# Optimization experiments

Measured on AMD Instinct MI355X. Metric: run time of the kernel, lower is better.

Reference implementation:

```python
import jax, jax.numpy as jnp
import numpy as np

B, S, D, H = 2, 2048, 1024, 16
HD = D // H  # head_dim = 64
SCALE = HD ** -0.5


def setup_inputs() -> dict:
    key = jax.random.key(0)
    ks = jax.random.split(key, 10)
    std = D ** -0.5
    return {
        "x": jax.random.normal(ks[0], (B, S, D), jnp.float32),
        "y": jax.random.normal(ks[1], (B, S, D), jnp.float32),
        "Wq": jax.random.normal(ks[2], (D, D), jnp.float32) * std,
        "bq": jnp.zeros((D,), jnp.float32),
        "Wk": jax.random.normal(ks[3], (D, D), jnp.float32) * std,
        "bk": jnp.zeros((D,), jnp.float32),
        "Wv": jax.random.normal(ks[4], (D, D), jnp.float32) * std,
        "bv": jnp.zeros((D,), jnp.float32),
        "Wo": jax.random.normal(ks[5], (D, D), jnp.float32) * std,
        "bo": jnp.zeros((D,), jnp.float32),
    }


def reference(x, y, Wq, bq, Wk, bk, Wv, bv, Wo, bo):
    # Linear projections (torch Linear: x @ W.T + b; here W stored as [in,out])
    q = x @ Wq + bq  # [B,S,D]
    k = y @ Wk + bk
    v = y @ Wv + bv
    # split heads -> [B,H,S,hd]
    q = q.reshape(B, S, H, HD).transpose(0, 2, 1, 3)
    k = k.reshape(B, S, H, HD).transpose(0, 2, 1, 3)
    v = v.reshape(B, S, H, HD).transpose(0, 2, 1, 3)
    scores = jnp.einsum("bhqd,bhkd->bhqk", q, k) * SCALE  # [B,H,S,S]
    causal = jnp.tril(jnp.ones((S, S), dtype=bool))  # keep lower triangle
    scores = jnp.where(causal[None, None], scores, -jnp.inf)
    attn = jax.nn.softmax(scores, axis=-1)
    out = jnp.einsum("bhqk,bhkd->bhqd", attn, v)  # [B,H,S,hd]
    out = out.transpose(0, 2, 1, 3).reshape(B, S, D)
    return out @ Wo + bo
```

## Files before the change

### kernel.cpp

```cpp
#include <hip/hip_runtime.h>
#include <hip/hip_bf16.h>


#define BDIM 2
#define SDIM 2048
#define DDIM 1024
#define HDIM 16
#define HD   64
#define MDIM (BDIM*SDIM)
#define C2 0.18033688011112042f

using short8  = __attribute__((ext_vector_type(8))) short;
using floatx4 = __attribute__((ext_vector_type(4))) float;

static __device__ __forceinline__ unsigned short f2bf(float x) {
    union { float f; unsigned int u; } c; c.f = x;
    unsigned int r = (c.u + 0x7fffu + ((c.u >> 16) & 1u)) >> 16;
    return (unsigned short)r;
}

static __device__ __forceinline__ unsigned int pack2bf(float a, float b) {
    union { float f; unsigned int u; } ua, ub;
    ua.f = a; ub.f = b;
    return __builtin_amdgcn_perm(ub.u + 0x8000u, ua.u + 0x8000u, 0x07060302u);
}

#define GLD16(g, l) __builtin_amdgcn_global_load_lds(                        \
    (const __attribute__((address_space(1))) void*)(g),                      \
    (__attribute__((address_space(3))) void*)(l), 16, 0, 0)

__global__ __launch_bounds__(256) void prep_kernel(
    const float* __restrict__ X, const float* __restrict__ Y,
    const float* __restrict__ W0, const float* __restrict__ W1,
    const float* __restrict__ W2, const float* __restrict__ W3,
    unsigned short* __restrict__ Xo, unsigned short* __restrict__ Yo,
    unsigned short* __restrict__ T0, unsigned short* __restrict__ T1,
    unsigned short* __restrict__ T2, unsigned short* __restrict__ T3)
{
    __shared__ float tile[64][68];
    const int z = blockIdx.z;
    const int t = threadIdx.x;
    if (z < 2) {
        const float* A    = z ? Y : X;
        unsigned short* O = z ? Yo : Xo;
        const int idx = blockIdx.x * 256 + t;
        const float4 a = ((const float4*)A)[idx*2];
        const float4 b = ((const float4*)A)[idx*2 + 1];
        ushort4 lo, hi;
        lo.x = f2bf(a.x); lo.y = f2bf(a.y); lo.z = f2bf(a.z); lo.w = f2bf(a.w);
        hi.x = f2bf(b.x); hi.y = f2bf(b.y); hi.z = f2bf(b.z); hi.w = f2bf(b.w);
        ((ushort4*)O)[idx*2]     = lo;
        ((ushort4*)O)[idx*2 + 1] = hi;
        return;
    }
    if (blockIdx.x >= 256) return;
    const int zz = z - 2;
    const float* W    = (zz == 0) ? W0 : (zz == 1) ? W1 : (zz == 2) ? W2 : W3;
    unsigned short* T = (zz == 0) ? T0 : (zz == 1) ? T1 : (zz == 2) ? T2 : T3;
    const int k0 = (blockIdx.x & 15) * 64, n0 = (blockIdx.x >> 4) * 64;
    #pragma unroll
    for (int i = 0; i < 4; ++i) {
        const int idx = t + i*256;
        const int kr = idx >> 4, c4 = idx & 15;
        float4 v = *(const float4*)&W[(size_t)(k0 + kr) * DDIM + n0 + c4*4];
        tile[kr][c4*4+0] = v.x; tile[kr][c4*4+1] = v.y;
        tile[kr][c4*4+2] = v.z; tile[kr][c4*4+3] = v.w;
    }
    __syncthreads();
    #pragma unroll
    for (int i = 0; i < 4; ++i) {
        const int idx = t + i*256;
        const int nr = idx >> 4, kc = idx & 15;
        ushort4 o;
        o.x = f2bf(tile[kc*4+0][nr]); o.y = f2bf(tile[kc*4+1][nr]);
        o.z = f2bf(tile[kc*4+2][nr]); o.w = f2bf(tile[kc*4+3][nr]);
        *(ushort4*)&T[(size_t)(n0 + nr) * DDIM + k0 + kc*4] = o;
    }
}

template <bool SWAP>
__device__ __forceinline__ void gemm128_core(
    const unsigned short* __restrict__ A, const unsigned short* __restrict__ Bt,
    int bm, int bn, unsigned short* As, unsigned short* Bs, floatx4 acc[4][4])
{
    const int t = threadIdx.x;
    const int w = t >> 6, l = t & 63;
    const int quad = l >> 4, col = l & 15;
    const int wr = (w >> 1) * 64, wc = (w & 1) * 64;

    const int c1 = t + 256;
    const int r0 = t >> 2,  o0 = (t & 3) * 8;
    const int r1 = c1 >> 2, o1 = (c1 & 3) * 8;

    const unsigned short* Ar0 = A  + (size_t)(bm + r0) * DDIM + o0;
    const unsigned short* Ar1 = A  + (size_t)(bm + r1) * DDIM + o1;
    const unsigned short* Br0 = Bt + (size_t)(bn + r0) * DDIM + o0;
    const unsigned short* Br1 = Bt + (size_t)(bn + r1) * DDIM + o1;

    GLD16(Ar0, As + t*8);
    GLD16(Ar1, As + c1*8);
    GLD16(Br0, Bs + t*8);
    GLD16(Br1, Bs + c1*8);

    for (int kt = 0; kt < DDIM; kt += 32) {
        const int cur = (kt >> 5) & 1;
        unsigned short* Asn = As + (cur ^ 1) * 4096;
        unsigned short* Bsn = Bs + (cur ^ 1) * 4096;
        __syncthreads();
        if (kt + 32 < DDIM) {
            GLD16(Ar0 + kt + 32, Asn + t*8);
            GLD16(Ar1 + kt + 32, Asn + c1*8);
            GLD16(Br0 + kt + 32, Bsn + t*8);
            GLD16(Br1 + kt + 32, Bsn + c1*8);
        }
        const unsigned short* Asc = As + cur*4096;
        const unsigned short* Bsc = Bs + cur*4096;
        short8 af[4], bfr[4];
        #pragma unroll
        for (int i = 0; i < 4; ++i)
            af[i] = *(const short8*)&Asc[(wr + i*16 + col)*32 + quad*8];
        #pragma unroll
        for (int j = 0; j < 4; ++j)
            bfr[j] = *(const short8*)&Bsc[(wc + j*16 + col)*32 + quad*8];
        #pragma unroll
        for (int i = 0; i < 4; ++i)
            #pragma unroll
            for (int j = 0; j < 4; ++j)
                acc[i][j] = SWAP
                    ? __builtin_amdgcn_mfma_f32_16x16x32_bf16(bfr[j], af[i], acc[i][j], 0, 0, 0)
                    : __builtin_amdgcn_mfma_f32_16x16x32_bf16(af[i], bfr[j], acc[i][j], 0, 0, 0);
    }
}

__global__ __launch_bounds__(256) void qkv_gemm_kernel(
    const unsigned short* __restrict__ xbf, const unsigned short* __restrict__ ybf,
    const unsigned short* __restrict__ Wqt, const unsigned short* __restrict__ Wkt,
    const unsigned short* __restrict__ Wvt,
    const float* __restrict__ bq, const float* __restrict__ bk,
    const float* __restrict__ bv,
    unsigned short* __restrict__ Qbf, unsigned short* __restrict__ Kbf,
    unsigned short* __restrict__ vT)
{
    __shared__ __align__(16) unsigned short As[2*4096];
    __shared__ __align__(16) unsigned short Bs[2*4096];

    const int z = blockIdx.z;
    const unsigned short* A  = (z == 0) ? xbf : ybf;
    const unsigned short* Wt = (z == 0) ? Wqt : (z == 1) ? Wkt : Wvt;
    const float* bp          = (z == 0) ? bq  : (z == 1) ? bk  : bv;

    const int bm = (blockIdx.x * 4 + (blockIdx.y & 3)) * 128;
    const int bn = (blockIdx.y >> 2) * 128;

    const int t = threadIdx.x;
    const int w = t >> 6, l = t & 63;
    const int quad = l >> 4, col = l & 15;
    const int wr = (w >> 1) * 64, wc = (w & 1) * 64;

    floatx4 acc[4][4] = {};

    if (z < 2) {
        gemm128_core<true>(A, Wt, bm, bn, As, Bs, acc);
        unsigned short* O = (z == 0) ? Qbf : Kbf;
        const float sc = (z == 0) ? C2 : 1.0f;
        float4 bias4[4];
        #pragma unroll
        for (int j = 0; j < 4; ++j)
            bias4[j] = *(const float4*)&bp[bn + wc + j*16 + quad*4];
        #pragma unroll
        for (int i = 0; i < 4; ++i) {
            const int m = bm + wr + i*16 + col;
            unsigned short* rowp = O + (size_t)m * DDIM;
            #pragma unroll
            for (int j = 0; j < 4; ++j) {
                const float v0 = (acc[i][j][0] + bias4[j].x) * sc;
                const float v1 = (acc[i][j][1] + bias4[j].y) * sc;
                const float v2 = (acc[i][j][2] + bias4[j].z) * sc;
                const float v3 = (acc[i][j][3] + bias4[j].w) * sc;
                uint2 pk;
                pk.x = pack2bf(v0, v1);
                pk.y = pack2bf(v2, v3);
                *(uint2*)&rowp[bn + wc + j*16 + quad*4] = pk;
            }
        }
    } else {
        gemm128_core<false>(A, Wt, bm, bn, As, Bs, acc);
        #pragma unroll
        for (int j = 0; j < 4; ++j) {
            const int gn = bn + wc + j*16 + col;
            const float bias = bp[gn];
            #pragma unroll
            for (int i = 0; i < 4; ++i) {
                const int gm0 = bm + wr + i*16 + quad*4;
                uint2 pk;
                pk.x = pack2bf(acc[i][j][0] + bias, acc[i][j][1] + bias);
                pk.y = pack2bf(acc[i][j][2] + bias, acc[i][j][3] + bias);
                *(uint2*)&vT[((size_t)((gm0 >> 11) * DDIM + gn)) * SDIM + (gm0 & 2047)] = pk;
            }
        }
    }
}

__global__ __launch_bounds__(256) void out_gemm_kernel(
    const unsigned short* __restrict__ Obf, const unsigned short* __restrict__ Wot,
    const float* __restrict__ bo, float* __restrict__ out)
{
    __shared__ __align__(16) unsigned short As[2*4096];
    __shared__ __align__(16) unsigned short Bs[2*2048];

    const int t = threadIdx.x;
    const int w = t >> 6, l = t & 63;
    const int quad = l >> 4, col = l & 15;

    const int j  = (blockIdx.x >> 3) + 2 * blockIdx.y;
    const int bm = ((blockIdx.x & 7) * 4 + (j & 3)) * 128;
    const int bn = (j >> 2) * 64;

    const int wr = (w >> 1) * 64, wc = (w & 1) * 32;

    const int r0 = t >> 2, o0 = (t & 3) * 8;
    const unsigned short* Ar0 = Obf + (size_t)(bm + r0) * DDIM + o0;
    const unsigned short* Ar1 = Obf + (size_t)(bm + 64 + r0) * DDIM + o0;
    const unsigned short* Br  = Wot + (size_t)(bn + r0) * DDIM + o0;

    floatx4 acc[4][2] = {};

    GLD16(Ar0, As + t*8);
    GLD16(Ar1, As + (t + 256)*8);
    GLD16(Br,  Bs + t*8);

    for (int kt = 0; kt < DDIM; kt += 32) {
        const int cur = (kt >> 5) & 1;
        unsigned short* Asn = As + (cur ^ 1) * 4096;
        unsigned short* Bsn = Bs + (cur ^ 1) * 2048;
        __syncthreads();
        if (kt + 32 < DDIM) {
            GLD16(Ar0 + kt + 32, Asn + t*8);
            GLD16(Ar1 + kt + 32, Asn + (t + 256)*8);
            GLD16(Br  + kt + 32, Bsn + t*8);
        }
        const unsigned short* Asc = As + cur*4096;
        const unsigned short* Bsc = Bs + cur*2048;
        short8 af[4], bfr[2];
        #pragma unroll
        for (int i = 0; i < 4; ++i)
            af[i] = *(const short8*)&Asc[(wr + i*16 + col)*32 + quad*8];
        #pragma unroll
        for (int j2 = 0; j2 < 2; ++j2)
            bfr[j2] = *(const short8*)&Bsc[(wc + j2*16 + col)*32 + quad*8];
        #pragma unroll
        for (int i = 0; i < 4; ++i)
            #pragma unroll
            for (int j2 = 0; j2 < 2; ++j2)
                acc[i][j2] = __builtin_amdgcn_mfma_f32_16x16x32_bf16(
                    bfr[j2], af[i], acc[i][j2], 0, 0, 0);
    }

    float4 bias4[2];
    #pragma unroll
    for (int j2 = 0; j2 < 2; ++j2)
        bias4[j2] = *(const float4*)&bo[bn + wc + j2*16 + quad*4];
    #pragma unroll
    for (int i = 0; i < 4; ++i) {
        const int m = bm + wr + i*16 + col;
        float* rowp = out + (size_t)m * DDIM;
        #pragma unroll
        for (int j2 = 0; j2 < 2; ++j2) {
            float4 o;
            o.x = acc[i][j2][0] + bias4[j2].x;
            o.y = acc[i][j2][1] + bias4[j2].y;
            o.z = acc[i][j2][2] + bias4[j2].z;
            o.w = acc[i][j2][3] + bias4[j2].w;
            *(float4*)&rowp[bn + wc + j2*16 + quad*4] = o;
        }
    }
}

__global__ __launch_bounds__(256) void attn_mfma_kernel(
    const unsigned short* __restrict__ Qbf, const unsigned short* __restrict__ Kbf,
    const unsigned short* __restrict__ vT, unsigned short* __restrict__ Obf)
{
    __shared__ __align__(16) unsigned short KfL[2][512*8];
    __shared__ __align__(16) unsigned short VfL[2][512*8];
    __shared__ __align__(16) unsigned short PfL[8*1024];

    const int t = threadIdx.x;
    const int w = t >> 6, l = t & 63;
    const int quad = l >> 4, col = l & 15;
    const int h  = blockIdx.x, b = blockIdx.z;
    const int qt = b ? (15 - blockIdx.y) : blockIdx.y;
    const size_t hoff = (size_t)h * HD;
    const size_t bS = (size_t)b * SDIM;
    const size_t bD = (size_t)b * DDIM;

    const int qwb = qt * 128 + w * 32;
    const int nk_block = 2*qt + 2;

    const unsigned short* kp[2];
    const unsigned short* vp[2];
    int kdst[2], vdst[2];
    #pragma unroll
    for (int i = 0; i < 2; ++i) {
        const int f = 2*w + i;
        kp[i]   = Kbf + (bS + (f >> 1)*16 + col) * DDIM + hoff + (f & 1)*32 + quad*8;
        vp[i]   = vT  + (bD + hoff + (f >> 1)*16 + col) * SDIM + (f & 1)*32 + quad*8;
        kdst[i] = (f*64 + l)*8;
        vdst[i] = (f*64 + l)*8;
    }

    short8 qf[2][2];
    #pragma unroll
    for (int qs = 0; qs < 2; ++qs)
        #pragma unroll
        for (int kc = 0; kc < 2; ++kc)
            qf[qs][kc] = *(const short8*)
                &Qbf[(bS + qwb + qs*16 + col) * DDIM + hoff + kc*32 + quad*8];

    float lrun[2] = {0.0f, 0.0f};
    floatx4 o[2][4] = {};

    #pragma unroll
    for (int i = 0; i < 2; ++i) {
        GLD16(kp[i], &KfL[0][kdst[i]]);
        GLD16(vp[i], &VfL[0][vdst[i]]);
    }

    #pragma unroll 1
    for (int it = 0; it < nk_block; ++it) {
        const int ktb = it * 64;
        const int cur = it & 1;
        __syncthreads();
        if (it + 1 < nk_block) {
            const int nxt = cur ^ 1;
            const size_t ko = (size_t)(it + 1) * 64 * DDIM;
            const int    vo = (it + 1) * 64;
            #pragma unroll
            for (int i = 0; i < 2; ++i) {
                GLD16(kp[i] + ko, &KfL[nxt][kdst[i]]);
                GLD16(vp[i] + vo, &VfL[nxt][vdst[i]]);
            }
        }
        if (ktb > qwb + 31) continue;

        const unsigned short* Kb = KfL[cur];
        const unsigned short* Vb = VfL[cur];
        short8 kf[4][2], vfr[4][2];
        #pragma unroll
        for (int kt = 0; kt < 4; ++kt)
            #pragma unroll
            for (int kc = 0; kc < 2; ++kc)
                kf[kt][kc] = *(const short8*)&Kb[((kt*2 + kc)*64 + l)*8];
        #pragma unroll
        for (int n = 0; n < 4; ++n)
            #pragma unroll
            for (int kk = 0; kk < 2; ++kk)
                vfr[n][kk] = *(const short8*)&Vb[((n*2 + kk)*64 + l)*8];

        #pragma unroll
        for (int qs = 0; qs < 2; ++qs) {
            if (ktb > qwb + qs*16 + 15) continue;

            floatx4 sT[4];
            #pragma unroll
            for (int kt = 0; kt < 4; ++kt) {
                floatx4 z = {};
                z = __builtin_amdgcn_mfma_f32_16x16x32_bf16(kf[kt][0], qf[qs][0], z, 0, 0, 0);
                z = __builtin_amdgcn_mfma_f32_16x16x32_bf16(kf[kt][1], qf[qs][1], z, 0, 0, 0);
                sT[kt] = z;
            }

            const int qrow = qwb + qs*16 + col;
            const bool anymask = (ktb + 63 > qwb + qs*16);
            float p[4][4];
            #pragma unroll
            for (int kt = 0; kt < 4; ++kt)
                #pragma unroll
                for (int r = 0; r < 4; ++r) {
                    float xv = sT[kt][r];
                    if (anymask && (ktb + kt*16 + quad*4 + r > qrow))
                        xv = -1e30f;
                    p[kt][r] = exp2f(xv);
                }

            float st[4];
            #pragma unroll
            for (int kt = 0; kt < 4; ++kt)
                st[kt] = (p[kt][0] + p[kt][1]) + (p[kt][2] + p[kt][3]);
            lrun[qs] += (st[0] + st[1]) + (st[2] + st[3]);

            const int pb = (w*2 + qs) * 1024;
            #pragma unroll
            for (int kt = 0; kt < 4; ++kt) {
                uint2 pk;
                pk.x = pack2bf(p[kt][0], p[kt][1]);
                pk.y = pack2bf(p[kt][2], p[kt][3]);
                *(uint2*)&PfL[pb + ((kt*2 + (quad>>1))*16 + col)*8 + (quad&1)*4] = pk;
            }
            const short8 pf0 = *(const short8*)&PfL[pb + ((0*4 + quad)*16 + col)*8];
            const short8 pf1 = *(const short8*)&PfL[pb + ((1*4 + quad)*16 + col)*8];
            #pragma unroll
            for (int n = 0; n < 4; ++n) {
                o[qs][n] = __builtin_amdgcn_mfma_f32_16x16x32_bf16(vfr[n][0], pf0, o[qs][n], 0, 0, 0);
                o[qs][n] = __builtin_amdgcn_mfma_f32_16x16x32_bf16(vfr[n][1], pf1, o[qs][n], 0, 0, 0);
            }
        }
    }

    #pragma unroll
    for (int qs = 0; qs < 2; ++qs) {
        float lt = lrun[qs];
        lt += __shfl_xor(lt, 16);
        lt += __shfl_xor(lt, 32);
        const float inv = 1.0f / lt;
        #pragma unroll
        for (int n = 0; n < 4; ++n) {
            ushort4 pk;
            pk.x = f2bf(o[qs][n][0] * inv); pk.y = f2bf(o[qs][n][1] * inv);
            pk.z = f2bf(o[qs][n][2] * inv); pk.w = f2bf(o[qs][n][3] * inv);
            *(ushort4*)&Obf[(bS + qwb + qs*16 + col) * DDIM + hoff + n*16 + quad*4] = pk;
        }
    }
}

extern "C" void kernel_launch(void* const* d_in, const int* in_sizes, int n_in,
                              void* d_out, int out_size, void* d_ws, size_t ws_size,
                              hipStream_t stream) {
    const float* x  = (const float*)d_in[0];
    const float* y  = (const float*)d_in[1];
    const float* Wq = (const float*)d_in[2];
    const float* bq = (const float*)d_in[3];
    const float* Wk = (const float*)d_in[4];
    const float* bk = (const float*)d_in[5];
    const float* Wv = (const float*)d_in[6];
    const float* bv = (const float*)d_in[7];
    const float* Wo = (const float*)d_in[8];
    const float* bo = (const float*)d_in[9];
    float* out = (float*)d_out;

    const size_t mat  = (size_t)MDIM * DDIM;
    const size_t wmat = (size_t)DDIM * DDIM;
    unsigned short* p = (unsigned short*)d_ws;
    unsigned short* xbf = p;            p += mat;
    unsigned short* ybf = p;            p += mat;
    unsigned short* Wqt = p;            p += wmat;
    unsigned short* Wkt = p;            p += wmat;
    unsigned short* Wvt = p;            p += wmat;
    unsigned short* Wot = p;            p += wmat;
    unsigned short* Qbf = p;            p += mat;
    unsigned short* Kbf = p;            p += mat;
    unsigned short* vT  = p;            p += mat;
    unsigned short* Obf = p;            p += mat;

    hipLaunchKernelGGL(prep_kernel, dim3(MDIM*DDIM/8/256, 1, 6), dim3(256),
                       0, stream, x, y, Wq, Wk, Wv, Wo,
                       xbf, ybf, Wqt, Wkt, Wvt, Wot);

    hipLaunchKernelGGL(qkv_gemm_kernel, dim3(DDIM/128, MDIM/128, 3), dim3(256),
                       0, stream, xbf, ybf, Wqt, Wkt, Wvt, bq, bk, bv,
                       Qbf, Kbf, vT);

    hipLaunchKernelGGL(attn_mfma_kernel, dim3(16, 16, BDIM), dim3(256),
                       0, stream, Qbf, Kbf, vT, Obf);

    hipLaunchKernelGGL(out_gemm_kernel, dim3(DDIM/64, MDIM/128), dim3(256),
                       0, stream, Obf, Wot, bo, out);
}
```

Before: 232.9 us.

## Halve attention query tile to 64 rows, doubling grid, add MFMA priority

The attention kernel now handles 64 query rows per block (16 per wave) instead of 128, doubling the grid to 16x32x2 blocks. Each wave keeps a single Q fragment and accumulator set, which cuts register use and the P scratch buffer, and launch bounds request 4 blocks per SIMD. The aim is more blocks and better occupancy and load balance on the causal triangle. s_setprio is also raised around the MFMA sections. The cost is that each K/V tile is loaded into LDS by twice as many blocks, raising global and LDS traffic.

```diff
diff --git a/kernel.cpp b/kernel.cpp
--- a/kernel.cpp
+++ b/kernel.cpp
@@ -276,25 +276,25 @@
     }
 }
 
-__global__ __launch_bounds__(256) void attn_mfma_kernel(
+__global__ __launch_bounds__(256, 4) void attn_mfma_kernel(
     const unsigned short* __restrict__ Qbf, const unsigned short* __restrict__ Kbf,
     const unsigned short* __restrict__ vT, unsigned short* __restrict__ Obf)
 {
     __shared__ __align__(16) unsigned short KfL[2][512*8];
     __shared__ __align__(16) unsigned short VfL[2][512*8];
-    __shared__ __align__(16) unsigned short PfL[8*1024];
+    __shared__ __align__(16) unsigned short PfL[4*1024];
 
     const int t = threadIdx.x;
     const int w = t >> 6, l = t & 63;
     const int quad = l >> 4, col = l & 15;
     const int h  = blockIdx.x, b = blockIdx.z;
-    const int qt = b ? (15 - blockIdx.y) : blockIdx.y;
+    const int qt = b ? (31 - blockIdx.y) : blockIdx.y;
     const size_t hoff = (size_t)h * HD;
     const size_t bS = (size_t)b * SDIM;
     const size_t bD = (size_t)b * DDIM;
 
-    const int qwb = qt * 128 + w * 32;
-    const int nk_block = 2*qt + 2;
+    const int qwb = qt * 64 + w * 16;
+    const int nk_block = qt + 1;
 
     const unsigned short* kp[2];
     const unsigned short* vp[2];
@@ -308,16 +308,14 @@
         vdst[i] = (f*64 + l)*8;
     }
 
-    short8 qf[2][2];
-    #pragma unroll
-    for (int qs = 0; qs < 2; ++qs)
-        #pragma unroll
-        for (int kc = 0; kc < 2; ++kc)
-            qf[qs][kc] = *(const short8*)
-                &Qbf[(bS + qwb + qs*16 + col) * DDIM + hoff + kc*32 + quad*8];
-
-    float lrun[2] = {0.0f, 0.0f};
-    floatx4 o[2][4] = {};
+    short8 qf[2];
+    #pragma unroll
+    for (int kc = 0; kc < 2; ++kc)
+        qf[kc] = *(const short8*)
+            &Qbf[(bS + qwb + col) * DDIM + hoff + kc*32 + quad*8];
+
+    float lrun = 0.0f;
+    floatx4 o[4] = {};
 
     #pragma unroll
     for (int i = 0; i < 2; ++i) {
@@ -340,7 +338,6 @@
                 GLD16(vp[i] + vo, &VfL[nxt][vdst[i]]);
             }
         }
-        if (ktb > qwb + 31) continue;
 
         const unsigned short* Kb = KfL[cur];
         const unsigned short* Vb = VfL[cur];
@@ -356,69 +353,65 @@
             for (int kk = 0; kk < 2; ++kk)
                 vfr[n][kk] = *(const short8*)&Vb[((n*2 + kk)*64 + l)*8];
 
-        #pragma unroll
-        for (int qs = 0; qs < 2; ++qs) {
-            if (ktb > qwb + qs*16 + 15) continue;
-
-            floatx4 sT[4];
-            #pragma unroll
-            for (int kt = 0; kt < 4; ++kt) {
-                floatx4 z = {};
-                z = __builtin_amdgcn_mfma_f32_16x16x32_bf16(kf[kt][0], qf[qs][0], z, 0, 0, 0);
-                z = __builtin_amdgcn_mfma_f32_16x16x32_bf16(kf[kt][1], qf[qs][1], z, 0, 0, 0);
-                sT[kt] = z;
+        floatx4 sT[4];
+        __builtin_amdgcn_s_setprio(1);
+        #pragma unroll
+        for (int kt = 0; kt < 4; ++kt) {
+            floatx4 z = {};
+            z = __builtin_amdgcn_mfma_f32_16x16x32_bf16(kf[kt][0], qf[0], z, 0, 0, 0);
+            z = __builtin_amdgcn_mfma_f32_16x16x32_bf16(kf[kt][1], qf[1], z, 0, 0, 0);
+            sT[kt] = z;
+        }
+        __builtin_amdgcn_s_setprio(0);
+
+        const int qrow = qwb + col;
+        const bool anymask = (ktb + 63 > qwb);
+        float p[4][4];
+        #pragma unroll
+        for (int kt = 0; kt < 4; ++kt)
+            #pragma unroll
+            for (int r = 0; r < 4; ++r) {
+                float xv = sT[kt][r];
+                if (anymask && (ktb + kt*16 + quad*4 + r > qrow))
+                    xv = -1e30f;
+                p[kt][r] = exp2f(xv);
             }
 
-            const int qrow = qwb + qs*16 + col;
-            const bool anymask = (ktb + 63 > qwb + qs*16);
-            float p[4][4];
-            #pragma unroll
-            for (int kt = 0; kt < 4; ++kt)
-                #pragma unroll
-                for (int r = 0; r < 4; ++r) {
-                    float xv = sT[kt][r];
-                    if (anymask && (ktb + kt*16 + quad*4 + r > qrow))
-                        xv = -1e30f;
-                    p[kt][r] = exp2f(xv);
-                }
-
-            float st[4];
-            #pragma unroll
-            for (int kt = 0; kt < 4; ++kt)
-                st[kt] = (p[kt][0] + p[kt][1]) + (p[kt][2] + p[kt][3]);
-            lrun[qs] += (st[0] + st[1]) + (st[2] + st[3]);
-
-            const int pb = (w*2 + qs) * 1024;
-            #pragma unroll
-            for (int kt = 0; kt < 4; ++kt) {
-                uint2 pk;
-                pk.x = pack2bf(p[kt][0], p[kt][1]);
-                pk.y = pack2bf(p[kt][2], p[kt][3]);
-                *(uint2*)&PfL[pb + ((kt*2 + (quad>>1))*16 + col)*8 + (quad&1)*4] = pk;
-            }
-            const short8 pf0 = *(const short8*)&PfL[pb + ((0*4 + quad)*16 + col)*8];
-            const short8 pf1 = *(const short8*)&PfL[pb + ((1*4 + quad)*16 + col)*8];
-            #pragma unroll
-            for (int n = 0; n < 4; ++n) {
-                o[qs][n] = __builtin_amdgcn_mfma_f32_16x16x32_bf16(vfr[n][0], pf0, o[qs][n], 0, 0, 0);
-                o[qs][n] = __builtin_amdgcn_mfma_f32_16x16x32_bf16(vfr[n][1], pf1, o[qs][n], 0, 0, 0);
-            }
-        }
-    }
-
-    #pragma unroll
-    for (int qs = 0; qs < 2; ++qs) {
-        float lt = lrun[qs];
-        lt += __shfl_xor(lt, 16);
-        lt += __shfl_xor(lt, 32);
-        const float inv = 1.0f / lt;
+        float st[4];
+        #pragma unroll
+        for (int kt = 0; kt < 4; ++kt)
+            st[kt] = (p[kt][0] + p[kt][1]) + (p[kt][2] + p[kt][3]);
+        lrun += (st[0] + st[1]) + (st[2] + st[3]);
+
+        const int pb = w * 1024;
+        #pragma unroll
+        for (int kt = 0; kt < 4; ++kt) {
+            uint2 pk;
+            pk.x = pack2bf(p[kt][0], p[kt][1]);
+            pk.y = pack2bf(p[kt][2], p[kt][3]);
+            *(uint2*)&PfL[pb + ((kt*2 + (quad>>1))*16 + col)*8 + (quad&1)*4] = pk;
+        }
+        const short8 pf0 = *(const short8*)&PfL[pb + ((0*4 + quad)*16 + col)*8];
+        const short8 pf1 = *(const short8*)&PfL[pb + ((1*4 + quad)*16 + col)*8];
+        __builtin_amdgcn_s_setprio(1);
         #pragma unroll
         for (int n = 0; n < 4; ++n) {
-            ushort4 pk;
-            pk.x = f2bf(o[qs][n][0] * inv); pk.y = f2bf(o[qs][n][1] * inv);
-            pk.z = f2bf(o[qs][n][2] * inv); pk.w = f2bf(o[qs][n][3] * inv);
-            *(ushort4*)&Obf[(bS + qwb + qs*16 + col) * DDIM + hoff + n*16 + quad*4] = pk;
-        }
+            o[n] = __builtin_amdgcn_mfma_f32_16x16x32_bf16(vfr[n][0], pf0, o[n], 0, 0, 0);
+            o[n] = __builtin_amdgcn_mfma_f32_16x16x32_bf16(vfr[n][1], pf1, o[n], 0, 0, 0);
+        }
+        __builtin_amdgcn_s_setprio(0);
+    }
+
+    float lt = lrun;
+    lt += __shfl_xor(lt, 16);
+    lt += __shfl_xor(lt, 32);
+    const float inv = 1.0f / lt;
+    #pragma unroll
+    for (int n = 0; n < 4; ++n) {
+        ushort4 pk;
+        pk.x = f2bf(o[n][0] * inv); pk.y = f2bf(o[n][1] * inv);
+        pk.z = f2bf(o[n][2] * inv); pk.w = f2bf(o[n][3] * inv);
+        *(ushort4*)&Obf[(bS + qwb + col) * DDIM + hoff + n*16 + quad*4] = pk;
     }
 }
 
@@ -459,7 +452,7 @@
                        0, stream, xbf, ybf, Wqt, Wkt, Wvt, bq, bk, bv,
                        Qbf, Kbf, vT);
 
-    hipLaunchKernelGGL(attn_mfma_kernel, dim3(16, 16, BDIM), dim3(256),
+    hipLaunchKernelGGL(attn_mfma_kernel, dim3(16, 32, BDIM), dim3(256),
                        0, stream, Qbf, Kbf, vT, Obf);
 
     hipLaunchKernelGGL(out_gemm_kernel, dim3(DDIM/64, MDIM/128), dim3(256),
```

Measured after the change: 218.2 us. 6.3% less time.
